# Kernel tuning notes

Hardware: AMD Instinct MI355X
Metric: run time of the kernel (lower is better)

## Reference

```python
import jax, jax.numpy as jnp
import numpy as np

N_LAYERS = 2
H_DIR = 200           # hidden_dim // 2 per direction
IN_SIZE = 400         # == hidden_dim
WORD_VOCAB, WORD_DIM = 100000, 300
POS_VOCAB, POS_DIM = 50, 100
SEQ = 512


def _lstm_dir(x, Wih, Whh, bih, bhh, reverse):
    # x: [n, in]; Wih: [4H, in]; Whh: [4H, H]; bih/bhh: [4H]
    H = Whh.shape[1]
    pre = x @ Wih.T + (bih + bhh)  # [n, 4H], hoist input projection out of scan

    def step(carry, p):
        h, c = carry
        g = p + h @ Whh.T
        i, f, gg, o = jnp.split(g, 4, axis=-1)  # torch gate order i,f,g,o
        i, f, o = jax.nn.sigmoid(i), jax.nn.sigmoid(f), jax.nn.sigmoid(o)
        c = f * c + i * jnp.tanh(gg)
        h = o * jnp.tanh(c)
        return (h, c), h

    init = (jnp.zeros((H,), x.dtype), jnp.zeros((H,), x.dtype))
    _, hs = jax.lax.scan(step, init, pre, reverse=reverse)
    return hs  # [n, H], aligned with input order


def setup_inputs() -> dict:
    key = jax.random.key(0)
    ks = jax.random.split(key, 20)
    s = 0.05
    inp = {}
    inp['word_emb'] = jax.random.normal(ks[0], (WORD_VOCAB, WORD_DIM), jnp.float32) * s
    inp['pos_emb'] = jax.random.normal(ks[1], (POS_VOCAB, POS_DIM), jnp.float32) * s
    # stacked LSTM params: [layer, direction, ...]; both layers have 400-dim input
    inp['Wih'] = jax.random.normal(ks[2], (N_LAYERS, 2, 4 * H_DIR, IN_SIZE), jnp.float32) * s
    inp['Whh'] = jax.random.normal(ks[3], (N_LAYERS, 2, 4 * H_DIR, H_DIR), jnp.float32) * s
    inp['bih'] = jax.random.normal(ks[4], (N_LAYERS, 2, 4 * H_DIR), jnp.float32) * s
    inp['bhh'] = jax.random.normal(ks[5], (N_LAYERS, 2, 4 * H_DIR), jnp.float32) * s
    inp['W_h1'] = jax.random.normal(ks[6], (IN_SIZE, IN_SIZE), jnp.float32) * s
    inp['b_h1'] = jax.random.normal(ks[7], (IN_SIZE,), jnp.float32) * s
    inp['W_h2'] = jax.random.normal(ks[8], (IN_SIZE, IN_SIZE), jnp.float32) * s
    inp['b_h2'] = jax.random.normal(ks[9], (IN_SIZE,), jnp.float32) * s
    inp['W_d1'] = jax.random.normal(ks[10], (IN_SIZE, IN_SIZE), jnp.float32) * s
    inp['b_d1'] = jax.random.normal(ks[11], (IN_SIZE,), jnp.float32) * s
    inp['W_d2'] = jax.random.normal(ks[12], (IN_SIZE, IN_SIZE), jnp.float32) * s
    inp['b_d2'] = jax.random.normal(ks[13], (IN_SIZE,), jnp.float32) * s
    inp['W_bi'] = jax.random.normal(ks[14], (IN_SIZE, IN_SIZE), jnp.float32) * s  # Bilinear weight [1,in,in] squeezed
    inp['b_bi'] = jax.random.normal(ks[15], (1,), jnp.float32) * s
    inp['sentence_word_indices'] = jax.random.randint(ks[16], (SEQ,), 0, WORD_VOCAB, jnp.int32)
    inp['sentence_pos_indices'] = jax.random.randint(ks[17], (SEQ,), 0, POS_VOCAB, jnp.int32)
    return inp


def reference(word_emb, pos_emb, Wih, Whh, bih, bhh,
              W_h1, b_h1, W_h2, b_h2, W_d1, b_d1, W_d2, b_d2,
              W_bi, b_bi, sentence_word_indices, sentence_pos_indices):
    # embedding lookup + concat -> [n, 400]
    x = jnp.concatenate([word_emb[sentence_word_indices],
                         pos_emb[sentence_pos_indices]], axis=1)
    # 2-layer bidirectional LSTM (batch=1, zero initial state)
    for l in range(N_LAYERS):
        fwd = _lstm_dir(x, Wih[l, 0], Whh[l, 0], bih[l, 0], bhh[l, 0], reverse=False)
        bwd = _lstm_dir(x, Wih[l, 1], Whh[l, 1], bih[l, 1], bhh[l, 1], reverse=True)
        x = jnp.concatenate([fwd, bwd], axis=-1)  # [n, 400]
    # batched head/dependent MLPs (original recomputes these per (i,j) pair)
    head = jax.nn.relu(jax.nn.relu(x @ W_h1.T + b_h1) @ W_h2.T + b_h2)  # [n, 400]
    dep = jax.nn.relu(jax.nn.relu(x @ W_d1.T + b_d1) @ W_d2.T + b_d2)   # [n, 400]
    # bilinear score matrix: score[i,j] = head_i^T W dep_j + b
    matrix = jnp.einsum('id,de,je->ij', head, W_bi, dep) + b_bi[0]  # [n, n]
    return matrix
```

## Files before the change

### kernel.cpp

```cpp
#include <hip/hip_runtime.h>
#include <hip/hip_bf16.h>
#include <cstdint>
#include <cstddef>


#define TSEQ 512
#define HDIR 200
#define INSZ 400
#define G4   800

typedef unsigned long long u64;

__global__ void k_embed(const float* __restrict__ we, const float* __restrict__ pe,
                        const int* __restrict__ wi, const int* __restrict__ pi,
                        float* __restrict__ x) {
  int t = blockIdx.x;
  int w = wi[t], p = pi[t];
  const float* wrow = we + (size_t)w * 300;
  const float* prow = pe + (size_t)p * 100;
  for (int j = threadIdx.x; j < INSZ; j += blockDim.x)
    x[(size_t)t * INSZ + j] = (j < 300) ? wrow[j] : prow[j - 300];
}

__global__ void k_add(const float* __restrict__ a, const float* __restrict__ b,
                      float* __restrict__ o, int n) {
  int i = blockIdx.x * blockDim.x + threadIdx.x;
  if (i < n) o[i] = a[i] + b[i];
}

__device__ __forceinline__ void gemm_bt_body(
    const float* __restrict__ A, const float* __restrict__ B,
    const float* __restrict__ bias, float* __restrict__ C,
    int m, int k, int bias_mode, int do_relu, int bx, int by)
{
  __shared__ float As[16][68];
  __shared__ float Bs[16][68];
  const int tid = threadIdx.x;
  const int tx = tid & 15, ty = tid >> 4;
  const int row0 = by << 6, col0 = bx << 6;
  const int lr = tid >> 2;
  const int kq = (tid & 3) << 2;
  float acc[4][4] = {};

  for (int ks = 0; ks < k; ks += 16) {
    float4 a4 = *(const float4*)(A + (size_t)(row0 + lr) * k + ks + kq);
    float4 b4 = make_float4(0.f, 0.f, 0.f, 0.f);
    if (col0 + lr < m)
      b4 = *(const float4*)(B + (size_t)(col0 + lr) * k + ks + kq);
    As[kq + 0][lr] = a4.x; As[kq + 1][lr] = a4.y; As[kq + 2][lr] = a4.z; As[kq + 3][lr] = a4.w;
    Bs[kq + 0][lr] = b4.x; Bs[kq + 1][lr] = b4.y; Bs[kq + 2][lr] = b4.z; Bs[kq + 3][lr] = b4.w;
    __syncthreads();
#pragma unroll
    for (int kk = 0; kk < 16; ++kk) {
      const float4 av = *(const float4*)&As[kk][ty << 2];
      const float4 bv = *(const float4*)&Bs[kk][tx << 2];
      const float a_[4] = {av.x, av.y, av.z, av.w};
      const float b_[4] = {bv.x, bv.y, bv.z, bv.w};
#pragma unroll
      for (int i = 0; i < 4; ++i)
#pragma unroll
        for (int j = 0; j < 4; ++j)
          acc[i][j] += a_[i] * b_[j];
    }
    __syncthreads();
  }

#pragma unroll
  for (int i = 0; i < 4; ++i) {
    const int r = row0 + (ty << 2) + i;
#pragma unroll
    for (int j = 0; j < 4; ++j) {
      const int c = col0 + (tx << 2) + j;
      if (c < m) {
        float v = acc[i][j];
        if (bias_mode == 1) v += bias[c];
        else if (bias_mode == 2) v += bias[0];
        if (do_relu) v = fmaxf(v, 0.f);
        C[(size_t)r * m + c] = v;
      }
    }
  }
}

__global__ __launch_bounds__(256) void k_gemm_bt(
    const float* __restrict__ A, const float* __restrict__ B,
    const float* __restrict__ bias, float* __restrict__ C,
    int m, int k, int bias_mode, int do_relu)
{
  gemm_bt_body(A, B, bias, C, m, k, bias_mode, do_relu, blockIdx.x, blockIdx.y);
}

__global__ __launch_bounds__(256) void k_gemm_bt_dual(
    const float* __restrict__ A0, const float* __restrict__ B0,
    const float* __restrict__ bias0, float* __restrict__ C0,
    const float* __restrict__ A1, const float* __restrict__ B1,
    const float* __restrict__ bias1, float* __restrict__ C1,
    int m, int k, int bias_mode, int do_relu)
{
  const float* A = blockIdx.z ? A1 : A0;
  const float* B = blockIdx.z ? B1 : B0;
  const float* bias = blockIdx.z ? bias1 : bias0;
  float* C = blockIdx.z ? C1 : C0;
  gemm_bt_body(A, B, bias, C, m, k, bias_mode, do_relu, blockIdx.x, blockIdx.y);
}

__global__ __launch_bounds__(448, 1) void k_scan(
    const float* __restrict__ Whh,
    const float* __restrict__ pre,
    float* __restrict__ hs,
    u64* hbuf,
    int layer)
{
  const int bid = blockIdx.x;
  if ((bid & 7) > 1) return;
  const int dir = bid & 7;
  const int p = bid >> 3;
  const int tid = threadIdx.x;
  const int rr = tid >> 1;
  const int u = tid & 1;
  const bool act = rr < HDIR;
  const int g = rr / 50;
  const int q = rr - g * 50;
  const int grow = act ? (g * HDIR + p * 50 + q) : 0;
  const int own0 = p * 50;

  __shared__ float h_lds[HDIR];
  __shared__ float g_lds[HDIR];

  float4 w[25];
  {
    const float* wrow = Whh + ((size_t)(layer * 2 + dir) * G4 + grow) * HDIR + u * 100;
#pragma unroll
    for (int i = 0; i < 25; ++i) w[i] = *(const float4*)(wrow + i * 4);
  }

  for (int i = tid; i < HDIR; i += 448) h_lds[i] = 0.f;
  float c_state = 0.f;
  u64* hb_dir = hbuf + dir * HDIR;
  __syncthreads();

  for (int t = 0; t < TSEQ; ++t) {
    const int inrow = dir ? (TSEQ - 1 - t) : t;

    float preval = 0.f;
    if (act && u == 0)
      preval = pre[(size_t)inrow * 1600 + dir * G4 + grow];

    if (t > 0 && tid < 150) {
      const int j = (tid < own0) ? tid : tid + 50;
      const u64* src = hb_dir + (size_t)(t & 1) * 400 + j;
      u64 v;
      do {
        v = __hip_atomic_load(src, __ATOMIC_RELAXED, __HIP_MEMORY_SCOPE_AGENT);
      } while ((unsigned)(v >> 32) < (unsigned)t);
      union { unsigned uu; float f; } cv; cv.uu = (unsigned)v;
      h_lds[j] = cv.f;
    }
    __syncthreads();

    if (act) {
      float4 acc = make_float4(0.f, 0.f, 0.f, 0.f);
      const float* hb = h_lds + u * 100;
#pragma unroll
      for (int i = 0; i < 25; ++i) {
        const float4 hv = *(const float4*)(hb + i * 4);
        acc.x += w[i].x * hv.x; acc.y += w[i].y * hv.y;
        acc.z += w[i].z * hv.z; acc.w += w[i].w * hv.w;
      }
      float tot = acc.x + acc.y + acc.z + acc.w;
      tot += __shfl_xor(tot, 1);
      if (u == 0) {
        const float gv = tot + preval;
        const float xx = (g == 2) ? 2.f * gv : gv;
        const float s = 1.f / (1.f + __expf(-xx));
        g_lds[rr] = (g == 2) ? (2.f * s - 1.f) : s;
      }
    }
    __syncthreads();

    if (tid < 50) {
      const float ai = g_lds[tid];
      const float af = g_lds[50 + tid];
      const float ag = g_lds[100 + tid];
      const float ao = g_lds[150 + tid];
      c_state = af * c_state + ai * ag;
      const float th = 2.f / (1.f + __expf(-2.f * c_state)) - 1.f;
      const float hv = ao * th;
      if (t != TSEQ - 1) {
        union { float f; unsigned uu; } cv; cv.f = hv;
        const u64 pk = ((u64)(unsigned)(t + 1) << 32) | cv.uu;
        __hip_atomic_store(hb_dir + (size_t)((t + 1) & 1) * 400 + own0 + tid,
                           pk, __ATOMIC_RELAXED, __HIP_MEMORY_SCOPE_AGENT);
      }
      h_lds[own0 + tid] = hv;
      hs[(size_t)inrow * INSZ + dir * HDIR + own0 + tid] = hv;
    }
  }
}

extern "C" void kernel_launch(void* const* d_in, const int* in_sizes, int n_in,
                              void* d_out, int out_size, void* d_ws, size_t ws_size,
                              hipStream_t stream)
{
  const float* we   = (const float*)d_in[0];
  const float* pe   = (const float*)d_in[1];
  const float* Wih  = (const float*)d_in[2];
  const float* Whh  = (const float*)d_in[3];
  const float* bih  = (const float*)d_in[4];
  const float* bhh  = (const float*)d_in[5];
  const float* W_h1 = (const float*)d_in[6];
  const float* b_h1 = (const float*)d_in[7];
  const float* W_h2 = (const float*)d_in[8];
  const float* b_h2 = (const float*)d_in[9];
  const float* W_d1 = (const float*)d_in[10];
  const float* b_d1 = (const float*)d_in[11];
  const float* W_d2 = (const float*)d_in[12];
  const float* b_d2 = (const float*)d_in[13];
  const float* W_bi = (const float*)d_in[14];
  const float* b_bi = (const float*)d_in[15];
  const int*   wi   = (const int*)d_in[16];
  const int*   pi   = (const int*)d_in[17];
  float* out = (float*)d_out;

  float* ws = (float*)d_ws;
  float* x0   = ws;
  float* pre  = ws + 204800;
  float* h1   = ws + 1024000;
  float* h2   = ws + 1228800;
  float* m1h  = ws + 1433600;
  float* m1d  = ws + 1638400;
  float* m2   = ws + 1843200;
  float* m3   = ws + 2048000;
  float* t1   = ws + 2252800;
  float* bsum = ws + 2457600;
  u64* hbuf0  = (u64*)(ws + 2461696);
  u64* hbuf1  = hbuf0 + 800;

  hipMemsetAsync(hbuf0, 0, 2 * 800 * sizeof(u64), stream);
  k_embed<<<TSEQ, 128, 0, stream>>>(we, pe, wi, pi, x0);
  k_add<<<(3200 + 255) / 256, 256, 0, stream>>>(bih, bhh, bsum, 3200);

  k_gemm_bt<<<dim3(25, 8), 256, 0, stream>>>(x0, Wih, bsum, pre, 1600, 400, 1, 0);
  k_scan<<<26, 448, 0, stream>>>(Whh, pre, h1, hbuf0, 0);
  k_gemm_bt<<<dim3(25, 8), 256, 0, stream>>>(h1, Wih + 1600 * 400, bsum + 1600, pre, 1600, 400, 1, 0);
  k_scan<<<26, 448, 0, stream>>>(Whh, pre, h2, hbuf1, 1);

  k_gemm_bt_dual<<<dim3(7, 8, 2), 256, 0, stream>>>(h2, W_h1, b_h1, m1h,
                                                    h2, W_d1, b_d1, m1d, 400, 400, 1, 1);
  k_gemm_bt_dual<<<dim3(7, 8, 2), 256, 0, stream>>>(m1h, W_h2, b_h2, m2,
                                                    m1d, W_d2, b_d2, m3, 400, 400, 1, 1);

  k_gemm_bt<<<dim3(7, 8), 256, 0, stream>>>(m3, W_bi, nullptr, t1, 400, 400, 0, 0);
  k_gemm_bt<<<dim3(8, 8), 256, 0, stream>>>(m2, t1, b_bi, out, 512, 400, 2, 0);
}
```

Before: 1.612 ms.

## Store LSTM recurrent weights as fp16 in LDS, one thread per gate row

```diff
diff --git a/kernel.cpp b/kernel.cpp
--- a/kernel.cpp
+++ b/kernel.cpp
@@ -1,5 +1,6 @@
 #include <hip/hip_runtime.h>
 #include <hip/hip_bf16.h>
+#include <hip/hip_fp16.h>
 #include <cstdint>
 #include <cstddef>
 
@@ -7,7 +8,6 @@
 #define TSEQ 512
 #define HDIR 200
 #define INSZ 400
-#define G4   800
 
 typedef unsigned long long u64;
 
@@ -104,77 +104,97 @@
   gemm_bt_body(A, B, bias, C, m, k, bias_mode, do_relu, blockIdx.x, blockIdx.y);
 }
 
-__global__ __launch_bounds__(448, 1) void k_scan(
-    const float* __restrict__ Whh,
-    const float* __restrict__ pre,
-    float* __restrict__ hs,
-    u64* hbuf,
-    int layer)
+__global__ __launch_bounds__(256)
+void k_scan(const float* __restrict__ Whh,
+            const float* __restrict__ pre,
+            float* __restrict__ hs,
+            u64* hbuf,
+            int layer)
 {
   const int bid = blockIdx.x;
   if ((bid & 7) > 1) return;
   const int dir = bid & 7;
   const int p = bid >> 3;
   const int tid = threadIdx.x;
-  const int rr = tid >> 1;
-  const int u = tid & 1;
-  const bool act = rr < HDIR;
-  const int g = rr / 50;
-  const int q = rr - g * 50;
-  const int grow = act ? (g * HDIR + p * 50 + q) : 0;
+  const bool act = tid < 200;
+  const int g = tid / 50;
+  const int q = tid - g * 50;
   const int own0 = p * 50;
-
-  __shared__ float h_lds[HDIR];
-  __shared__ float g_lds[HDIR];
-
-  float4 w[25];
-  {
-    const float* wrow = Whh + ((size_t)(layer * 2 + dir) * G4 + grow) * HDIR + u * 100;
-#pragma unroll
-    for (int i = 0; i < 25; ++i) w[i] = *(const float4*)(wrow + i * 4);
-  }
-
-  for (int i = tid; i < HDIR; i += 448) h_lds[i] = 0.f;
+  const int grow = g * HDIR + own0 + q;
+
+  extern __shared__ float smem[];
+  char* w_base = (char*)smem;
+  float* h_lds = smem + 20000;
+  float* g_lds = h_lds + HDIR;
+
+  const float* WhhL = Whh + (size_t)(layer * 2 + dir) * 800 * 200;
+  u64* hb_dir = hbuf + dir * HDIR;
+
+  for (int idx = tid; idx < 200 * 25; idx += 256) {
+    const int lr = idx / 25;
+    const int c8 = idx - lr * 25;
+    const int gg = lr / 50, qq = lr - gg * 50;
+    const float* src = WhhL + ((size_t)(gg * HDIR + own0 + qq)) * HDIR + c8 * 8;
+    const float4 v0 = *(const float4*)(src);
+    const float4 v1 = *(const float4*)(src + 4);
+    const __half2 p0 = __floats2half2_rn(v0.x, v0.y);
+    const __half2 p1 = __floats2half2_rn(v0.z, v0.w);
+    const __half2 p2 = __floats2half2_rn(v1.x, v1.y);
+    const __half2 p3 = __floats2half2_rn(v1.z, v1.w);
+    uint4 pk;
+    pk.x = *reinterpret_cast<const unsigned*>(&p0);
+    pk.y = *reinterpret_cast<const unsigned*>(&p1);
+    pk.z = *reinterpret_cast<const unsigned*>(&p2);
+    pk.w = *reinterpret_cast<const unsigned*>(&p3);
+    *(uint4*)(w_base + c8 * 3200 + lr * 16) = pk;
+  }
+  for (int i = tid; i < HDIR; i += 256) h_lds[i] = 0.f;
   float c_state = 0.f;
-  u64* hb_dir = hbuf + dir * HDIR;
   __syncthreads();
 
+#pragma unroll 1
   for (int t = 0; t < TSEQ; ++t) {
     const int inrow = dir ? (TSEQ - 1 - t) : t;
+    const int par = t & 1;
 
     float preval = 0.f;
-    if (act && u == 0)
-      preval = pre[(size_t)inrow * 1600 + dir * G4 + grow];
+    if (act)
+      preval = pre[(size_t)inrow * 1600 + dir * 800 + grow];
 
     if (t > 0 && tid < 150) {
       const int j = (tid < own0) ? tid : tid + 50;
-      const u64* src = hb_dir + (size_t)(t & 1) * 400 + j;
-      u64 v;
-      do {
-        v = __hip_atomic_load(src, __ATOMIC_RELAXED, __HIP_MEMORY_SCOPE_AGENT);
-      } while ((unsigned)(v >> 32) < (unsigned)t);
+      const u64* s = hb_dir + (size_t)par * 400 + j;
+      u64 v = __hip_atomic_load(s, __ATOMIC_RELAXED, __HIP_MEMORY_SCOPE_AGENT);
+      int guard = 0;
+      while ((unsigned)(v >> 32) < (unsigned)t && ++guard < (1 << 18))
+        v = __hip_atomic_load(s, __ATOMIC_RELAXED, __HIP_MEMORY_SCOPE_AGENT);
       union { unsigned uu; float f; } cv; cv.uu = (unsigned)v;
       h_lds[j] = cv.f;
     }
     __syncthreads();
 
     if (act) {
-      float4 acc = make_float4(0.f, 0.f, 0.f, 0.f);
-      const float* hb = h_lds + u * 100;
-#pragma unroll
-      for (int i = 0; i < 25; ++i) {
-        const float4 hv = *(const float4*)(hb + i * 4);
-        acc.x += w[i].x * hv.x; acc.y += w[i].y * hv.y;
-        acc.z += w[i].z * hv.z; acc.w += w[i].w * hv.w;
+      unsigned roff = (unsigned)tid * 16u;
+      asm volatile("" : "+v"(roff));
+      float a0 = 0.f, a1 = 0.f, a2 = 0.f, a3 = 0.f;
+#pragma unroll
+      for (int c = 0; c < 25; ++c) {
+        const uint4 wq = *(const uint4*)(w_base + c * 3200 + roff);
+        const float4 h0 = *(const float4*)(h_lds + c * 8);
+        const float4 h1 = *(const float4*)(h_lds + c * 8 + 4);
+        const float2 f0 = __half22float2(*reinterpret_cast<const __half2*>(&wq.x));
+        const float2 f1 = __half22float2(*reinterpret_cast<const __half2*>(&wq.y));
+        const float2 f2 = __half22float2(*reinterpret_cast<const __half2*>(&wq.z));
+        const float2 f3 = __half22float2(*reinterpret_cast<const __half2*>(&wq.w));
+        a0 += f0.x * h0.x + f2.x * h1.x;
+        a1 += f0.y * h0.y + f2.y * h1.y;
+        a2 += f1.x * h0.z + f3.x * h1.z;
+        a3 += f1.y * h0.w + f3.y * h1.w;
       }
-      float tot = acc.x + acc.y + acc.z + acc.w;
-      tot += __shfl_xor(tot, 1);
-      if (u == 0) {
-        const float gv = tot + preval;
-        const float xx = (g == 2) ? 2.f * gv : gv;
-        const float s = 1.f / (1.f + __expf(-xx));
-        g_lds[rr] = (g == 2) ? (2.f * s - 1.f) : s;
-      }
+      const float gv = (a0 + a1) + (a2 + a3) + preval;
+      const float xx = (g == 2) ? 2.f * gv : gv;
+      const float s = 1.f / (1.f + __expf(-xx));
+      g_lds[tid] = (g == 2) ? (2.f * s - 1.f) : s;
     }
     __syncthreads();
 
@@ -236,14 +256,18 @@
   u64* hbuf0  = (u64*)(ws + 2461696);
   u64* hbuf1  = hbuf0 + 800;
 
+  const int SMEM = 80000 + 2 * HDIR * 4;
+  hipFuncSetAttribute((const void*)k_scan,
+                      hipFuncAttributeMaxDynamicSharedMemorySize, SMEM);
+
   hipMemsetAsync(hbuf0, 0, 2 * 800 * sizeof(u64), stream);
   k_embed<<<TSEQ, 128, 0, stream>>>(we, pe, wi, pi, x0);
   k_add<<<(3200 + 255) / 256, 256, 0, stream>>>(bih, bhh, bsum, 3200);
 
   k_gemm_bt<<<dim3(25, 8), 256, 0, stream>>>(x0, Wih, bsum, pre, 1600, 400, 1, 0);
-  k_scan<<<26, 448, 0, stream>>>(Whh, pre, h1, hbuf0, 0);
+  k_scan<<<32, 256, SMEM, stream>>>(Whh, pre, h1, hbuf0, 0);
   k_gemm_bt<<<dim3(25, 8), 256, 0, stream>>>(h1, Wih + 1600 * 400, bsum + 1600, pre, 1600, 400, 1, 0);
-  k_scan<<<26, 448, 0, stream>>>(Whh, pre, h2, hbuf1, 1);
+  k_scan<<<32, 256, SMEM, stream>>>(Whh, pre, h2, hbuf1, 1);
 
   k_gemm_bt_dual<<<dim3(7, 8, 2), 256, 0, stream>>>(h2, W_h1, b_h1, m1h,
                                                     h2, W_d1, b_d1, m1d, 400, 400, 1, 1);
```

Measured after the change: 2.751 ms. 1.71x slower.
